# Performance work log

Measured on AMD Instinct MI355X. Metric: run time of the kernel, lower is better.

Reference implementation:

```python
import jax, jax.numpy as jnp
import numpy as np


def setup_inputs() -> dict:
    key = jax.random.key(0)
    k1, k2, k3, k4 = jax.random.split(key, 4)
    B, S, D, Hd = 4, 4096, 1024, 128
    x = jax.random.normal(k1, (B, S, D), dtype=jnp.float32)
    # nn.Linear(D, Hd, bias=False) weight has shape [Hd, D]; we store transposed [D, Hd]
    scale = 1.0 / np.sqrt(D)
    Wq = jax.random.normal(k2, (D, Hd), dtype=jnp.float32) * scale
    Wk = jax.random.normal(k3, (D, Hd), dtype=jnp.float32) * scale
    Wv = jax.random.normal(k4, (D, Hd), dtype=jnp.float32) * scale
    return {"x": x, "Wq": Wq, "Wk": Wk, "Wv": Wv}


def reference(x, Wq, Wk, Wv):
    # Q/K/V projections: [B,S,D] @ [D,Hd] -> [B,S,Hd]
    Q = jnp.einsum("bsd,dh->bsh", x, Wq)
    K = jnp.einsum("bsd,dh->bsh", x, Wk)
    V = jnp.einsum("bsd,dh->bsh", x, Wv)
    head_dim = K.shape[-1]
    inv_sqrt = jnp.asarray(1.0 / np.sqrt(head_dim), dtype=Q.dtype)
    # full [B,S,S] scores (matches the original non-fused implementation)
    scores = jnp.einsum("bqh,bkh->bqk", Q, K) * inv_sqrt
    attn = jax.nn.softmax(scores, axis=-1)
    out = jnp.einsum("bqk,bkh->bqh", attn, V)
    return out
```

## Files before the change

### kernel.cpp

```cpp
#include <hip/hip_runtime.h>


#define BB 4
#define SS 4096
#define DD 1024
#define HDIM 128
#define NTIL 16
#define KVB 64

typedef _Float16 f16;
typedef _Float16 half8 __attribute__((ext_vector_type(8)));
typedef _Float16 half4 __attribute__((ext_vector_type(4)));
typedef __fp16 fp16x2 __attribute__((ext_vector_type(2)));
typedef float f32x4 __attribute__((ext_vector_type(4)));

__device__ __forceinline__ void gload_lds16(const void* g, void* l) {
  __builtin_amdgcn_global_load_lds(
      (const __attribute__((address_space(1))) void*)g,
      (__attribute__((address_space(3))) void*)l, 16, 0, 0);
}

__device__ __forceinline__ f32x4 mfma16(half8 a, half8 b, f32x4 c) {
  return __builtin_amdgcn_mfma_f32_16x16x32_f16(a, b, c, 0, 0, 0);
}

__global__ void wt_kernel(const float* __restrict__ Wq, const float* __restrict__ Wk,
                          const float* __restrict__ Wv, f16* __restrict__ w3t) {
  const int n = blockIdx.x;
  const float* W = (n < 128) ? Wq : (n < 256) ? Wk : Wv;
  const int col = n & 127;
  for (int d = threadIdx.x; d < DD; d += blockDim.x)
    w3t[(size_t)n * DD + d] = (f16)W[(size_t)d * HDIM + col];
}

__global__ __launch_bounds__(256, 2) void proj_kernel(
    const float* __restrict__ x, const f16* __restrict__ w3t,
    f16* __restrict__ Qm, f16* __restrict__ Km, f16* __restrict__ VTm) {
  __shared__ __align__(16) float xa[2][32 * 32];
  const int tid = threadIdx.x;
  const int lane = tid & 63;
  const int wid = tid >> 6;
  const int lo = lane & 15, hi = lane >> 4;
  const int row0 = blockIdx.x * 32;

  auto STAGE = [&](int kc, int bufsel) {
    const int r = tid >> 3, c4 = tid & 7;
    gload_lds16((const char*)(x + (size_t)(row0 + r) * DD + kc * 32) +
                    ((c4 * 16) ^ ((r & 7) << 4)),
                (char*)&xa[bufsel][0] + wid * 1024);
  };

  f32x4 acc[2][6];
#pragma unroll
  for (int m = 0; m < 2; ++m)
#pragma unroll
    for (int nf = 0; nf < 6; ++nf) acc[m][nf] = (f32x4){0.f, 0.f, 0.f, 0.f};

  STAGE(0, 0);
  int cur = 0;
#pragma unroll 1
  for (int kc = 0; kc < 32; ++kc) {
    if (kc + 1 < 32) {
      STAGE(kc + 1, cur ^ 1);
      asm volatile("s_waitcnt vmcnt(1)" ::: "memory");
    } else {
      asm volatile("s_waitcnt vmcnt(0)" ::: "memory");
    }
    __builtin_amdgcn_s_barrier();

    const char* xb = (const char*)&xa[cur][0];
    const int k0 = kc * 32 + hi * 8;
    half8 af[2];
#pragma unroll
    for (int m = 0; m < 2; ++m) {
      const int row = m * 16 + lo;
      const int base = row * 128 + hi * 32;
      const int swz = (row & 7) << 4;
      f32x4 a0 = *(const f32x4*)(xb + (base ^ swz));
      f32x4 a1 = *(const f32x4*)(xb + ((base + 16) ^ swz));
      union { fp16x2 h2[4]; half8 h8; } u;
      u.h2[0] = __builtin_amdgcn_cvt_pkrtz(a0[0], a0[1]);
      u.h2[1] = __builtin_amdgcn_cvt_pkrtz(a0[2], a0[3]);
      u.h2[2] = __builtin_amdgcn_cvt_pkrtz(a1[0], a1[1]);
      u.h2[3] = __builtin_amdgcn_cvt_pkrtz(a1[2], a1[3]);
      af[m] = u.h8;
    }
#pragma unroll
    for (int nf = 0; nf < 6; ++nf) {
      const int n = wid * 96 + nf * 16 + lo;
      half8 bf = *(const half8*)(w3t + (size_t)n * DD + k0);
      acc[0][nf] = mfma16(af[0], bf, acc[0][nf]);
      acc[1][nf] = mfma16(af[1], bf, acc[1][nf]);
    }
    __builtin_amdgcn_s_barrier();
    cur ^= 1;
  }

#pragma unroll
  for (int m = 0; m < 2; ++m) {
#pragma unroll
    for (int nf = 0; nf < 6; ++nf) {
      const int n = wid * 96 + nf * 16 + lo;
#pragma unroll
      for (int r = 0; r < 4; ++r) {
        const int row = row0 + m * 16 + hi * 4 + r;
        const f16 v = (f16)acc[m][nf][r];
        if (n < 128) {
          Qm[(size_t)row * HDIM + n] = v;
        } else if (n < 256) {
          Km[(size_t)row * HDIM + (n - 128)] = v;
        } else {
          const int b = row >> 12, s = row & 4095;
          const int t = s & 31;
          const int sp = (s & ~31) | ((t & 0x0C) << 1) | ((t & 0x10) >> 2) | (t & 3);
          VTm[((size_t)b * HDIM + (n - 256)) * SS + sp] = v;
        }
      }
    }
  }
}

__global__ __launch_bounds__(512)
__attribute__((amdgpu_waves_per_eu(2, 2)))
void attn_kernel(
    const f16* __restrict__ Qm, const f16* __restrict__ Km,
    const f16* __restrict__ VTm, float* __restrict__ out,
    float* __restrict__ lws) {
  __shared__ __align__(16) f16 Kt[2][KVB * 128];
  __shared__ __align__(16) f16 Vt[2][128 * KVB];

  const int xcd = blockIdx.x & 7;
  const int idx = blockIdx.x >> 3;
  const int group = xcd * 2 + (idx >> 4);
  const int b = group >> 2;
  const int split = group & 3;
  const int qt = idx & 15;
  const int tid = threadIdx.x;
  const int wid = tid >> 6;
  const int lane = tid & 63;
  const int lo = lane & 15, hi = lane >> 4;
  const int q0 = qt * 256 + wid * 32;
  const int kbase = split * (NTIL * KVB);

  constexpr float SCL2E = 0.12751744560817508f;

  half8 qf[2][4];
#pragma unroll
  for (int m = 0; m < 2; ++m)
#pragma unroll
    for (int c = 0; c < 4; ++c) {
      half8 q = *(const half8*)(Qm + (size_t)(b * SS + q0 + m * 16 + lo) * HDIM +
                                c * 32 + hi * 8);
#pragma unroll
      for (int j = 0; j < 8; ++j) q[j] = (f16)((float)q[j] * SCL2E);
      qf[m][c] = q;
    }

  f32x4 of[2][8];
#pragma unroll
  for (int m = 0; m < 2; ++m)
#pragma unroll
    for (int g2 = 0; g2 < 8; ++g2) of[m][g2] = (f32x4){0.f, 0.f, 0.f, 0.f};
  float lrun[2] = {0.f, 0.f};

  const char* kgb = (const char*)(Km + ((size_t)b * SS + kbase) * HDIM);
  const char* vgb = (const char*)(VTm + (size_t)b * HDIM * SS) + (size_t)kbase * 2;

  auto STAGE = [&](int kt2, int bufsel) {
    char* kd = (char*)&Kt[bufsel][0];
    char* vd = (char*)&Vt[bufsel][0];
#pragma unroll
    for (int i = 0; i < 2; ++i) {
      const int cid = i * 512 + tid;
      const int r = cid >> 4, c4 = cid & 15;
      gload_lds16(kgb + (size_t)(kt2 * KVB + r) * 256 + ((c4 * 16) ^ ((r & 7) << 4)),
                  kd + (size_t)(i * 512 + wid * 64) * 16);
    }
#pragma unroll
    for (int i = 0; i < 2; ++i) {
      const int cid = i * 512 + tid;
      const int r = cid >> 3, c8 = cid & 7;
      gload_lds16(vgb + (size_t)r * (SS * 2) + (size_t)(kt2 * KVB) * 2 +
                      ((c8 * 16) ^ ((r & 7) << 4)),
                  vd + (size_t)(i * 512 + wid * 64) * 16);
    }
  };

  STAGE(0, 0);
  int cur = 0;
#pragma unroll 1
  for (int kt = 0; kt < NTIL; ++kt) {
    if (kt + 1 < NTIL) {
      STAGE(kt + 1, cur ^ 1);
      asm volatile("s_waitcnt vmcnt(4)" ::: "memory");
    } else {
      asm volatile("s_waitcnt vmcnt(0)" ::: "memory");
    }
    __builtin_amdgcn_s_barrier();

    const char* KtC = (const char*)&Kt[cur][0];
    const char* VtC = (const char*)&Vt[cur][0];

    f32x4 sc[2][4];
#pragma unroll
    for (int m = 0; m < 2; ++m)
#pragma unroll
      for (int g = 0; g < 4; ++g) sc[m][g] = (f32x4){0.f, 0.f, 0.f, 0.f};
#pragma unroll
    for (int c = 0; c < 4; ++c)
#pragma unroll
      for (int g = 0; g < 4; ++g) {
        const int row = g * 16 + lo;
        const half8 kb = *(const half8*)(KtC + row * 256 +
                                         ((c * 64 + hi * 16) ^ ((row & 7) << 4)));
        sc[0][g] = mfma16(kb, qf[0][c], sc[0][g]);
        sc[1][g] = mfma16(kb, qf[1][c], sc[1][g]);
      }

    half8 pa[2][2];
#pragma unroll
    for (int m = 0; m < 2; ++m) {
#pragma unroll
      for (int kc = 0; kc < 2; ++kc) {
        union { half4 h4[2]; half8 h8; } pu;
#pragma unroll
        for (int gg = 0; gg < 2; ++gg) {
          const int g = kc * 2 + gg;
          const float p0 = __builtin_amdgcn_exp2f(sc[m][g][0]);
          const float p1 = __builtin_amdgcn_exp2f(sc[m][g][1]);
          const float p2 = __builtin_amdgcn_exp2f(sc[m][g][2]);
          const float p3 = __builtin_amdgcn_exp2f(sc[m][g][3]);
          union { fp16x2 h2[2]; half4 h4; } u;
          u.h2[0] = __builtin_amdgcn_cvt_pkrtz(p0, p1);
          u.h2[1] = __builtin_amdgcn_cvt_pkrtz(p2, p3);
          pu.h4[gg] = u.h4;
          lrun[m] += (p0 + p1) + (p2 + p3);
        }
        pa[m][kc] = pu.h8;
      }
    }

#pragma unroll
    for (int kc = 0; kc < 2; ++kc)
#pragma unroll
      for (int g2 = 0; g2 < 8; ++g2) {
        const int row = g2 * 16 + lo;
        const half8 vb = *(const half8*)(VtC + row * 128 +
                                         ((kc * 64 + hi * 16) ^ ((row & 7) << 4)));
        of[0][g2] = mfma16(pa[0][kc], vb, of[0][g2]);
        of[1][g2] = mfma16(pa[1][kc], vb, of[1][g2]);
      }

    __builtin_amdgcn_s_barrier();
    cur ^= 1;
  }

#pragma unroll
  for (int m = 0; m < 2; ++m) {
    lrun[m] += __shfl_xor(lrun[m], 16, 64);
    lrun[m] += __shfl_xor(lrun[m], 32, 64);
  }

  float* op = out + ((size_t)(b * SS + q0)) * HDIM;
#pragma unroll
  for (int m = 0; m < 2; ++m) {
#pragma unroll
    for (int r = 0; r < 4; ++r) {
      const int row = m * 16 + hi * 4 + r;
#pragma unroll
      for (int g2 = 0; g2 < 8; ++g2)
        atomicAdd(&op[(size_t)row * HDIM + g2 * 16 + lo], of[m][g2][r]);
    }
  }
  if (hi == 0) {
    atomicAdd(&lws[b * SS + q0 + lo], lrun[0]);
    atomicAdd(&lws[b * SS + q0 + 16 + lo], lrun[1]);
  }
}

__global__ void norm_kernel(float* __restrict__ out, const float* __restrict__ lws) {
  const int idx = blockIdx.x * 256 + threadIdx.x;
  f32x4 v = ((const f32x4*)out)[idx];
  const float inv = 1.0f / lws[idx >> 5];
  v[0] *= inv; v[1] *= inv; v[2] *= inv; v[3] *= inv;
  ((f32x4*)out)[idx] = v;
}

extern "C" void kernel_launch(void* const* d_in, const int* in_sizes, int n_in,
                              void* d_out, int out_size, void* d_ws, size_t ws_size,
                              hipStream_t stream) {
  (void)in_sizes; (void)n_in; (void)out_size; (void)ws_size;
  const float* x  = (const float*)d_in[0];
  const float* Wq = (const float*)d_in[1];
  const float* Wk = (const float*)d_in[2];
  const float* Wv = (const float*)d_in[3];
  float* out = (float*)d_out;

  f16* Qm  = (f16*)d_ws;
  f16* Km  = Qm + (size_t)BB * SS * HDIM;
  f16* VTm = Km + (size_t)BB * SS * HDIM;
  f16* W3  = VTm + (size_t)BB * SS * HDIM;
  float* lws = (float*)(W3 + (size_t)384 * DD);

  hipMemsetAsync(out, 0, (size_t)BB * SS * HDIM * sizeof(float), stream);
  hipMemsetAsync(lws, 0, (size_t)BB * SS * sizeof(float), stream);

  hipLaunchKernelGGL(wt_kernel, dim3(384), dim3(256), 0, stream, Wq, Wk, Wv, W3);
  hipLaunchKernelGGL(proj_kernel, dim3(512), dim3(256), 0, stream, x, W3, Qm, Km, VTm);
  hipLaunchKernelGGL(attn_kernel, dim3(256), dim3(512), 0, stream, Qm, Km, VTm, out, lws);
  hipLaunchKernelGGL(norm_kernel, dim3(2048), dim3(256), 0, stream, out, lws);
}
```

Before: 132.6 us.

## Double projection row tile and software-pipeline weight fragment loads in registers

The projection kernel now processes 64 rows per block instead of 32, so each weight fragment loaded from global memory feeds four MFMAs instead of two and fewer blocks are launched. Weight fragments for the next k-chunk are prefetched into a second register set while the current chunk computes, with the loop unrolled by two and the waitcnt thresholds adjusted for the extra in-flight loads. Occupancy is pinned to one wave per EU to allow the larger accumulator and prefetch register footprint. The trade-off is fewer blocks (256) over the 256 CUs and less latency hiding from other waves.

```diff
diff --git a/kernel.cpp b/kernel.cpp
--- a/kernel.cpp
+++ b/kernel.cpp
@@ -33,46 +33,60 @@
     w3t[(size_t)n * DD + d] = (f16)W[(size_t)d * HDIM + col];
 }
 
-__global__ __launch_bounds__(256, 2) void proj_kernel(
+__global__ __launch_bounds__(256)
+__attribute__((amdgpu_waves_per_eu(1, 1)))
+void proj_kernel(
     const float* __restrict__ x, const f16* __restrict__ w3t,
     f16* __restrict__ Qm, f16* __restrict__ Km, f16* __restrict__ VTm) {
-  __shared__ __align__(16) float xa[2][32 * 32];
+  __shared__ __align__(16) float xa[2][64 * 32];
   const int tid = threadIdx.x;
   const int lane = tid & 63;
   const int wid = tid >> 6;
   const int lo = lane & 15, hi = lane >> 4;
-  const int row0 = blockIdx.x * 32;
+  const int row0 = blockIdx.x * 64;
 
   auto STAGE = [&](int kc, int bufsel) {
-    const int r = tid >> 3, c4 = tid & 7;
-    gload_lds16((const char*)(x + (size_t)(row0 + r) * DD + kc * 32) +
-                    ((c4 * 16) ^ ((r & 7) << 4)),
-                (char*)&xa[bufsel][0] + wid * 1024);
+#pragma unroll
+    for (int i = 0; i < 2; ++i) {
+      const int cid = i * 256 + tid;
+      const int r = cid >> 3, c4 = cid & 7;
+      gload_lds16((const char*)(x + (size_t)(row0 + r) * DD + kc * 32) +
+                      ((c4 * 16) ^ ((r & 7) << 4)),
+                  (char*)&xa[bufsel][0] + (size_t)(i * 256 + wid * 64) * 16);
+    }
   };
 
-  f32x4 acc[2][6];
-#pragma unroll
-  for (int m = 0; m < 2; ++m)
+  half8 bfA[6], bfB[6];
+  auto BLOAD = [&](half8 (&bf)[6], int kc) {
+#pragma unroll
+    for (int nf = 0; nf < 6; ++nf) {
+      const int n = wid * 96 + nf * 16 + lo;
+      bf[nf] = *(const half8*)(w3t + (size_t)n * DD + kc * 32 + hi * 8);
+    }
+  };
+
+  f32x4 acc[4][6];
+#pragma unroll
+  for (int m = 0; m < 4; ++m)
 #pragma unroll
     for (int nf = 0; nf < 6; ++nf) acc[m][nf] = (f32x4){0.f, 0.f, 0.f, 0.f};
 
-  STAGE(0, 0);
-  int cur = 0;
-#pragma unroll 1
-  for (int kc = 0; kc < 32; ++kc) {
+  auto ITER = [&](int kc, int cur, half8 (&bfCur)[6], half8 (&bfNext)[6]) {
     if (kc + 1 < 32) {
       STAGE(kc + 1, cur ^ 1);
-      asm volatile("s_waitcnt vmcnt(1)" ::: "memory");
+      asm volatile("s_waitcnt vmcnt(8)" ::: "memory");
     } else {
-      asm volatile("s_waitcnt vmcnt(0)" ::: "memory");
+      asm volatile("s_waitcnt vmcnt(6)" ::: "memory");
     }
     __builtin_amdgcn_s_barrier();
 
+    if (kc + 1 < 32) BLOAD(bfNext, kc + 1);
+    __builtin_amdgcn_sched_barrier(0);
+
     const char* xb = (const char*)&xa[cur][0];
-    const int k0 = kc * 32 + hi * 8;
-    half8 af[2];
-#pragma unroll
-    for (int m = 0; m < 2; ++m) {
+    half8 af[4];
+#pragma unroll
+    for (int m = 0; m < 4; ++m) {
       const int row = m * 16 + lo;
       const int base = row * 128 + hi * 32;
       const int swz = (row & 7) << 4;
@@ -86,18 +100,24 @@
       af[m] = u.h8;
     }
 #pragma unroll
-    for (int nf = 0; nf < 6; ++nf) {
-      const int n = wid * 96 + nf * 16 + lo;
-      half8 bf = *(const half8*)(w3t + (size_t)n * DD + k0);
-      acc[0][nf] = mfma16(af[0], bf, acc[0][nf]);
-      acc[1][nf] = mfma16(af[1], bf, acc[1][nf]);
-    }
+    for (int nf = 0; nf < 6; ++nf)
+#pragma unroll
+      for (int m = 0; m < 4; ++m)
+        acc[m][nf] = mfma16(af[m], bfCur[nf], acc[m][nf]);
+
     __builtin_amdgcn_s_barrier();
-    cur ^= 1;
-  }
-
-#pragma unroll
-  for (int m = 0; m < 2; ++m) {
+  };
+
+  STAGE(0, 0);
+  BLOAD(bfA, 0);
+#pragma unroll 1
+  for (int kc = 0; kc < 32; kc += 2) {
+    ITER(kc, 0, bfA, bfB);
+    ITER(kc + 1, 1, bfB, bfA);
+  }
+
+#pragma unroll
+  for (int m = 0; m < 4; ++m) {
 #pragma unroll
     for (int nf = 0; nf < 6; ++nf) {
       const int n = wid * 96 + nf * 16 + lo;
@@ -306,7 +326,7 @@
   hipMemsetAsync(lws, 0, (size_t)BB * SS * sizeof(float), stream);
 
   hipLaunchKernelGGL(wt_kernel, dim3(384), dim3(256), 0, stream, Wq, Wk, Wv, W3);
-  hipLaunchKernelGGL(proj_kernel, dim3(512), dim3(256), 0, stream, x, W3, Qm, Km, VTm);
+  hipLaunchKernelGGL(proj_kernel, dim3(256), dim3(256), 0, stream, x, W3, Qm, Km, VTm);
   hipLaunchKernelGGL(attn_kernel, dim3(256), dim3(512), 0, stream, Qm, Km, VTm, out, lws);
   hipLaunchKernelGGL(norm_kernel, dim3(2048), dim3(256), 0, stream, out, lws);
 }
```

Result: faster. 119.6 us (-9.8%).
